# Kernel tuning notes

Measured on AMD Instinct MI355X. Metric: run time of the kernel, lower is better.

Reference implementation:

```python
import jax, jax.numpy as jnp
import numpy as np

N = 50000      # nodes
E = 800000     # edges (avg degree 16)
D_IN, D_H, D_OUT = 128, 128, 64


def setup_inputs() -> dict:
    key = jax.random.key(0)
    ks = jax.random.split(key, 12)
    s = 0.05  # weight init scale
    return {
        "x": jax.random.normal(ks[0], (N, D_IN), jnp.float32),
        "edge_index": jax.random.randint(ks[1], (2, E), 0, N, dtype=jnp.int64),
        "Wl0": jax.random.normal(ks[2], (D_H, D_IN), jnp.float32) * s,
        "bl0": jax.random.normal(ks[3], (D_H,), jnp.float32) * s,
        "Wr0": jax.random.normal(ks[4], (D_H, D_IN), jnp.float32) * s,
        "Wl1": jax.random.normal(ks[5], (D_H, D_H), jnp.float32) * s,
        "bl1": jax.random.normal(ks[6], (D_H,), jnp.float32) * s,
        "Wr1": jax.random.normal(ks[7], (D_H, D_H), jnp.float32) * s,
        "Wl2": jax.random.normal(ks[8], (D_OUT, D_H), jnp.float32) * s,
        "bl2": jax.random.normal(ks[9], (D_OUT,), jnp.float32) * s,
        "Wr2": jax.random.normal(ks[10], (D_OUT, D_H), jnp.float32) * s,
    }


def _sage_layer(h, src, dst, Wl, bl, Wr):
    # mean aggregation over incoming neighbors: out[i] = mean_{j in N(i)} h[j]
    n = h.shape[0]
    agg = jax.ops.segment_sum(h[src], dst, num_segments=n)          # [N, D]
    deg = jax.ops.segment_sum(jnp.ones((src.shape[0],), h.dtype), dst,
                              num_segments=n)                        # [N]
    mean = agg / jnp.maximum(deg, 1.0)[:, None]  # empty rows -> 0, matches torch_sparse
    # lin_l(agg) + lin_r(self); lin_r has no bias in PyG SAGEConv
    return mean @ Wl.T + bl + h @ Wr.T


def reference(x, edge_index, Wl0, bl0, Wr0, Wl1, bl1, Wr1, Wl2, bl2, Wr2):
    src, dst = edge_index[1], edge_index[0]  # adj row = dst, col = src
    h = jax.nn.relu(_sage_layer(x, src, dst, Wl0, bl0, Wr0))
    h = jax.nn.relu(_sage_layer(h, src, dst, Wl1, bl1, Wr1))
    h = _sage_layer(h, src, dst, Wl2, bl2, Wr2)
    return jax.nn.log_softmax(h, axis=1)
```

## Files before the change

kernel.cpp:

```cpp
#include <hip/hip_runtime.h>
#include <hip/hip_bf16.h>


typedef __attribute__((ext_vector_type(8))) short bf16x8;
typedef __attribute__((ext_vector_type(4))) float f32x4;

#define NPB 128
#define BCAP 2560
#define EPB 8192
#define EPT 32
#define CPAD 16

__device__ __forceinline__ unsigned short f2bf(float f) {
    unsigned int u = __builtin_bit_cast(unsigned int, f);
    u += 0x7fffu + ((u >> 16) & 1u);
    return (unsigned short)(u >> 16);
}
__device__ __forceinline__ float bf2f(unsigned int bits16) {
    return __builtin_bit_cast(float, bits16 << 16);
}


__global__ __launch_bounds__(256) void dist_cast_kernel(const int* __restrict__ dst,
                                                        const int* __restrict__ srcv,
                                                        int* __restrict__ gcnt,
                                                        unsigned int* __restrict__ staging,
                                                        int E, int NBc, int DB, int XB,
                                                        const float* __restrict__ x,
                                                        unsigned short* __restrict__ xbf,
                                                        const float* p0, const float* p1,
                                                        const float* p2, const float* p3,
                                                        const float* p4, const float* p5,
                                                        unsigned short* __restrict__ wbf) {
    __shared__ unsigned int stage[EPB];
    __shared__ int hist[400];
    __shared__ int lstart[400];
    __shared__ int gbase[400];
    __shared__ int scanbuf[256];
    int bid = blockIdx.x;
    int t = threadIdx.x;

    if (bid >= DB && bid < DB + XB) {
        int base = (bid - DB) * 256 + t;
        int stride = XB * 256;
        const float2* x2 = (const float2*)x;
        unsigned int* xo = (unsigned int*)xbf;
#pragma unroll
        for (int k = 0; k < 4; ++k) {
            int idx = base + k * stride;
            float2 v = x2[idx];
            xo[idx] = (unsigned int)f2bf(v.x) | ((unsigned int)f2bf(v.y) << 16);
        }
        return;
    }
    if (bid >= DB + XB) {
        int w = (bid - DB - XB) * 256 + t;
        if (w < 40960) {
            const float* src;
            int local;
            if      (w < 8192)  { src = p0; local = w; }
            else if (w < 16384) { src = p1; local = w - 8192; }
            else if (w < 24576) { src = p2; local = w - 16384; }
            else if (w < 32768) { src = p3; local = w - 24576; }
            else if (w < 36864) { src = p4; local = w - 32768; }
            else                { src = p5; local = w - 36864; }
            float2 v = ((const float2*)src)[local];
            unsigned int p = (unsigned int)f2bf(v.x) | ((unsigned int)f2bf(v.y) << 16);
            ((unsigned int*)wbf)[w] = p;
        }
        return;
    }

    int e0 = bid * EPB;
    unsigned int w[EPT];

    for (int b = t; b < NBc + 1; b += 256) hist[b] = 0;
    __syncthreads();

#pragma unroll
    for (int i = 0; i < EPT; ++i) {
        int e = e0 + i * 256 + t;
        unsigned int word = 0xFFFFFFFFu;
        if (e < E) word = ((unsigned int)dst[e] << 16) | (unsigned int)srcv[e];
        w[i] = word;
        int b = (int)(word >> 23); if (b > NBc) b = NBc;
        atomicAdd(&hist[b], 1);
    }
    __syncthreads();

    int b0 = 2 * t, b1 = 2 * t + 1;
    int h0 = (b0 <= NBc) ? hist[b0] : 0;
    int h1 = (b1 <= NBc) ? hist[b1] : 0;
    int pair = h0 + h1;
    scanbuf[t] = pair;
    __syncthreads();
    for (int off = 1; off < 256; off <<= 1) {
        int v = (t >= off) ? scanbuf[t - off] : 0;
        __syncthreads();
        scanbuf[t] += v;
        __syncthreads();
    }
    int excl = scanbuf[t] - pair;
    if (b0 <= NBc) lstart[b0] = excl;
    if (b1 <= NBc) lstart[b1] = excl + h0;
    __syncthreads();

    for (int b = t; b < NBc; b += 256) {
        int h = hist[b];
        gbase[b] = h ? atomicAdd(&gcnt[b * CPAD], h) : 0;
    }
    for (int b = t; b < NBc + 1; b += 256) hist[b] = lstart[b];
    __syncthreads();

#pragma unroll
    for (int i = 0; i < EPT; ++i) {
        unsigned int word = w[i];
        int b = (int)(word >> 23); if (b > NBc) b = NBc;
        int p = atomicAdd(&hist[b], 1);
        stage[p] = word;
    }
    __syncthreads();

    int total = lstart[NBc];
    for (int i = t; i < total; i += 256) {
        unsigned int word = stage[i];
        int b = (int)(word >> 23);
        int gpos = gbase[b] + (i - lstart[b]);
        staging[(size_t)b * BCAP + gpos] = word;
    }
}


template<int GY>
__device__ __forceinline__ void gemm_body(int mb, int y,
                                          const unsigned short* __restrict__ H,
                                          const unsigned short* __restrict__ Wl,
                                          const unsigned short* __restrict__ Wr,
                                          unsigned short* __restrict__ C, int N) {
    __shared__ unsigned short clds[4 * 32 * 68];
    const int NCOL = GY * 64;
    const int half = GY >> 1;
    int wave = threadIdx.x >> 6;
    int lane = threadIdx.x & 63;
    int l15 = lane & 15, quad = lane >> 4;
    const unsigned short* W = (y < half) ? Wl : Wr;
    int wrow0 = (y < half ? y : y - half) * 64;
    int col0 = y * 64;
    int m0 = mb * 128 + wave * 32;

    int r0 = m0 + l15;      if (r0 > N - 1) r0 = N - 1;
    int r1 = m0 + 16 + l15; if (r1 > N - 1) r1 = N - 1;
    const bf16x8* A0 = (const bf16x8*)(H + (size_t)r0 * 128);
    const bf16x8* A1 = (const bf16x8*)(H + (size_t)r1 * 128);

    f32x4 acc[2][4] = {};
#pragma unroll
    for (int ks = 0; ks < 4; ++ks) {
        int vidx = ks * 4 + quad;
        bf16x8 a0 = A0[vidx];
        bf16x8 a1 = A1[vidx];
#pragma unroll
        for (int j = 0; j < 4; ++j) {
            const bf16x8* B = (const bf16x8*)(W + (size_t)(wrow0 + j * 16 + l15) * 128);
            bf16x8 b = B[vidx];
            acc[0][j] = __builtin_amdgcn_mfma_f32_16x16x32_bf16(a0, b, acc[0][j], 0, 0, 0);
            acc[1][j] = __builtin_amdgcn_mfma_f32_16x16x32_bf16(a1, b, acc[1][j], 0, 0, 0);
        }
    }

    unsigned short* slice = clds + wave * (32 * 68);
#pragma unroll
    for (int i = 0; i < 2; ++i)
#pragma unroll
        for (int j = 0; j < 4; ++j)
#pragma unroll
            for (int r = 0; r < 4; ++r)
                slice[(i * 16 + quad * 4 + r) * 68 + j * 16 + l15] = f2bf(acc[i][j][r]);
    __syncthreads();

    int rlo = lane >> 3, j8 = lane & 7;
#pragma unroll
    for (int pass = 0; pass < 4; ++pass) {
        int row_local = pass * 8 + rlo;
        const unsigned short* p = slice + row_local * 68 + j8 * 8;
        unsigned long long lo = *(const unsigned long long*)(p);
        unsigned long long hi = *(const unsigned long long*)(p + 4);
        int row = m0 + row_local;
        if (row < N) {
            unsigned long long* q = (unsigned long long*)(C + (size_t)row * NCOL + col0 + j8 * 8);
            q[0] = lo;
            q[1] = hi;
        }
    }
}


__global__ __launch_bounds__(256) void build_gemm_kernel(const unsigned int* __restrict__ staging,
                                                         const int* __restrict__ gcnt,
                                                         int* __restrict__ row_ptr,
                                                         int* __restrict__ adj, int N, int NBc,
                                                         int gemmRows,
                                                         const unsigned short* __restrict__ H,
                                                         const unsigned short* __restrict__ Wl,
                                                         const unsigned short* __restrict__ Wr,
                                                         unsigned short* __restrict__ C) {
    __shared__ int hist[NPB];
    __shared__ int scn[NPB];
    __shared__ int wsum[4];
    int bid = blockIdx.x;
    int t = threadIdx.x;

    if (bid >= NBc) {
        int gid = bid - NBc;
        int mb = gid % gemmRows;
        int yy = gid / gemmRows;
        gemm_body<4>(mb, yy, H, Wl, Wr, C, N);
        return;
    }

    int b = bid;
    int n0 = b * NPB;
    int nb = N - n0; if (nb > NPB) nb = NPB;
    int ec = gcnt[b * CPAD];
    const unsigned int* st = staging + (size_t)b * BCAP;

    int a = 0;
    for (int j = t; j < b; j += 256) a += gcnt[j * CPAD];
#pragma unroll
    for (int off = 32; off; off >>= 1) a += __shfl_xor(a, off);
    if ((t & 63) == 0) wsum[t >> 6] = a;
    if (t < NPB) hist[t] = 0;
    __syncthreads();
    int bb = wsum[0] + wsum[1] + wsum[2] + wsum[3];

    for (int i = t; i < ec; i += 256)
        atomicAdd(&hist[(st[i] >> 16) & (NPB - 1)], 1);
    __syncthreads();

    int v = (t < NPB) ? hist[t] : 0;
    if (t < NPB) scn[t] = v;
    __syncthreads();
    for (int off = 1; off < NPB; off <<= 1) {
        int u = (t >= off && t < NPB) ? scn[t - off] : 0;
        __syncthreads();
        if (t < NPB) scn[t] += u;
        __syncthreads();
    }
    if (t < NPB) hist[t] = scn[t] - v;
    if (t < nb) row_ptr[n0 + t] = bb + (scn[t] - v);
    if (b == NBc - 1 && t == 0) row_ptr[N] = bb + ec;
    __syncthreads();

    for (int i = t; i < ec; i += 256) {
        unsigned int pk = st[i];
        int p = atomicAdd(&hist[(pk >> 16) & (NPB - 1)], 1);
        adj[bb + p] = (int)(pk & 0xffffu);
    }
}


template<int GY>
__global__ __launch_bounds__(256) void gemm_mfma_kernel(const unsigned short* __restrict__ H,
                                                        const unsigned short* __restrict__ Wl,
                                                        const unsigned short* __restrict__ Wr,
                                                        unsigned short* __restrict__ C,
                                                        int N) {
    gemm_body<GY>(blockIdx.x, blockIdx.y, H, Wl, Wr, C, N);
}


__global__ __launch_bounds__(256) void agg_relu_kernel(const unsigned short* __restrict__ C,
                                                       const int* __restrict__ row_ptr,
                                                       const int* __restrict__ adj,
                                                       const float* __restrict__ bias,
                                                       unsigned short* __restrict__ hout, int N) {
    int node = (int)((blockIdx.x * blockDim.x + threadIdx.x) >> 6);
    int lane = threadIdx.x & 63;
    if (node >= N) return;
    int g = lane >> 4;
    int c = lane & 15;
    int beg = row_ptr[node], end = row_ptr[node + 1];
    float p[8] = {};

    int e = beg;
    while (e < end) {
        int cnt = end - e; if (cnt > 64) cnt = 64;
        int ll = lane; if (ll > cnt - 1) ll = cnt - 1;
        int myidx = adj[e + ll];
        int c1 = cnt - 1;
        for (int i = 0; i < cnt; i += 16) {
            int t0 = i + g, t1 = i + 4 + g, t2 = i + 8 + g, t3 = i + 12 + g;
            int s0 = __shfl(myidx, t0 > c1 ? c1 : t0);
            int s1 = __shfl(myidx, t1 > c1 ? c1 : t1);
            int s2 = __shfl(myidx, t2 > c1 ? c1 : t2);
            int s3 = __shfl(myidx, t3 > c1 ? c1 : t3);
            float m0 = t0 < cnt ? 1.f : 0.f;
            float m1 = t1 < cnt ? 1.f : 0.f;
            float m2 = t2 < cnt ? 1.f : 0.f;
            float m3 = t3 < cnt ? 1.f : 0.f;
            bf16x8 v0 = ((const bf16x8*)(C + (size_t)s0 * 256))[c];
            bf16x8 v1 = ((const bf16x8*)(C + (size_t)s1 * 256))[c];
            bf16x8 v2 = ((const bf16x8*)(C + (size_t)s2 * 256))[c];
            bf16x8 v3 = ((const bf16x8*)(C + (size_t)s3 * 256))[c];
#pragma unroll
            for (int k = 0; k < 8; ++k) {
                p[k] += m0 * bf2f((unsigned short)v0[k]);
                p[k] += m1 * bf2f((unsigned short)v1[k]);
                p[k] += m2 * bf2f((unsigned short)v2[k]);
                p[k] += m3 * bf2f((unsigned short)v3[k]);
            }
        }
        e += cnt;
    }

#pragma unroll
    for (int k = 0; k < 8; ++k) {
        p[k] += __shfl_xor(p[k], 16);
        p[k] += __shfl_xor(p[k], 32);
    }

    int deg = end - beg;
    float inv = 1.0f / (float)(deg > 1 ? deg : 1);
    bf16x8 sv = ((const bf16x8*)(C + (size_t)node * 256))[16 + c];
    float4 b0 = ((const float4*)bias)[2 * c];
    float4 b1 = ((const float4*)bias)[2 * c + 1];
    float bb[8] = {b0.x, b0.y, b0.z, b0.w, b1.x, b1.y, b1.z, b1.w};
    bf16x8 o;
#pragma unroll
    for (int k = 0; k < 8; ++k) {
        float v = fmaxf(p[k] * inv + bb[k] + bf2f((unsigned short)sv[k]), 0.f);
        o[k] = (short)f2bf(v);
    }
    if (g == 0)
        ((bf16x8*)(hout + (size_t)node * 128))[c] = o;
}


__global__ __launch_bounds__(256) void final_kernel(const unsigned short* __restrict__ C,
                                                    const int* __restrict__ row_ptr,
                                                    const int* __restrict__ adj,
                                                    const float* __restrict__ bias,
                                                    float* __restrict__ out, int N) {
    int node = (int)((blockIdx.x * blockDim.x + threadIdx.x) >> 6);
    int lane = threadIdx.x & 63;
    if (node >= N) return;
    int g = lane >> 3;
    int c = lane & 7;
    int beg = row_ptr[node], end = row_ptr[node + 1];
    float p[8] = {};

    int e = beg;
    while (e < end) {
        int cnt = end - e; if (cnt > 64) cnt = 64;
        int ll = lane; if (ll > cnt - 1) ll = cnt - 1;
        int myidx = adj[e + ll];
        int c1 = cnt - 1;
        for (int i = 0; i < cnt; i += 16) {
            int ta = i + g, tb = i + 8 + g;
            int sa = __shfl(myidx, ta > c1 ? c1 : ta);
            int sb = __shfl(myidx, tb > c1 ? c1 : tb);
            float ma = ta < cnt ? 1.f : 0.f;
            float mb = tb < cnt ? 1.f : 0.f;
            bf16x8 va = ((const bf16x8*)(C + (size_t)sa * 128))[c];
            bf16x8 vb = ((const bf16x8*)(C + (size_t)sb * 128))[c];
#pragma unroll
            for (int k = 0; k < 8; ++k) {
                p[k] += ma * bf2f((unsigned short)va[k]);
                p[k] += mb * bf2f((unsigned short)vb[k]);
            }
        }
        e += cnt;
    }

#pragma unroll
    for (int k = 0; k < 8; ++k) {
        p[k] += __shfl_xor(p[k], 8);
        p[k] += __shfl_xor(p[k], 16);
        p[k] += __shfl_xor(p[k], 32);
    }

    int deg = end - beg;
    float inv = 1.0f / (float)(deg > 1 ? deg : 1);
    bf16x8 sv = ((const bf16x8*)(C + (size_t)node * 128))[8 + c];
    float4 b0 = ((const float4*)bias)[2 * c];
    float4 b1 = ((const float4*)bias)[2 * c + 1];
    float bb[8] = {b0.x, b0.y, b0.z, b0.w, b1.x, b1.y, b1.z, b1.w};
    float u[8];
#pragma unroll
    for (int k = 0; k < 8; ++k)
        u[k] = p[k] * inv + bb[k] + bf2f((unsigned short)sv[k]);

    float m = u[0];
#pragma unroll
    for (int k = 1; k < 8; ++k) m = fmaxf(m, u[k]);
#pragma unroll
    for (int off = 1; off < 8; off <<= 1) m = fmaxf(m, __shfl_xor(m, off));
    float se = 0.f;
#pragma unroll
    for (int k = 0; k < 8; ++k) se += __expf(u[k] - m);
#pragma unroll
    for (int off = 1; off < 8; off <<= 1) se += __shfl_xor(se, off);
    float ls = __logf(se);

    if (g == 0) {
        float4 o0 = {u[0] - m - ls, u[1] - m - ls, u[2] - m - ls, u[3] - m - ls};
        float4 o1 = {u[4] - m - ls, u[5] - m - ls, u[6] - m - ls, u[7] - m - ls};
        ((float4*)(out + (size_t)node * 64))[2 * c] = o0;
        ((float4*)(out + (size_t)node * 64))[2 * c + 1] = o1;
    }
}


extern "C" void kernel_launch(void* const* d_in, const int* in_sizes, int n_in,
                              void* d_out, int out_size, void* d_ws, size_t ws_size,
                              hipStream_t stream) {
    const float* x   = (const float*)d_in[0];
    const int*   ei  = (const int*)d_in[1];
    const float* Wl0 = (const float*)d_in[2];
    const float* bl0 = (const float*)d_in[3];
    const float* Wr0 = (const float*)d_in[4];
    const float* Wl1 = (const float*)d_in[5];
    const float* bl1 = (const float*)d_in[6];
    const float* Wr1 = (const float*)d_in[7];
    const float* Wl2 = (const float*)d_in[8];
    const float* bl2 = (const float*)d_in[9];
    const float* Wr2 = (const float*)d_in[10];
    float* out = (float*)d_out;

    const int N  = in_sizes[0] / 128;
    const int E  = in_sizes[1] / 2;
    const int NB = (N + NPB - 1) / NPB;

    char* ws = (char*)d_ws;
    auto alloc = [&](size_t bytes) {
        char* p = ws;
        ws += (bytes + 255) & ~(size_t)255;
        return p;
    };
    int*   row_ptr    = (int*)alloc((size_t)(N + 1) * 4);
    int*   adj        = (int*)alloc((size_t)E * 4);
    int*   gcnt       = (int*)alloc((size_t)NB * CPAD * 4);
    unsigned int* staging = (unsigned int*)alloc((size_t)NB * BCAP * 4);
    unsigned short* xbf = (unsigned short*)alloc((size_t)N * 128 * 2);
    unsigned short* wbf = (unsigned short*)alloc((size_t)81920 * 2);
    unsigned short* C   = (unsigned short*)alloc((size_t)N * 256 * 2);
    unsigned short* hA  = (unsigned short*)alloc((size_t)N * 128 * 2);
    unsigned short* hB  = (unsigned short*)alloc((size_t)N * 128 * 2);

    const int* dstp = ei;
    const int* srcp = ei + E;

    unsigned short* wl0 = wbf;
    unsigned short* wr0 = wbf + 16384;
    unsigned short* wl1 = wbf + 32768;
    unsigned short* wr1 = wbf + 49152;
    unsigned short* wl2 = wbf + 65536;
    unsigned short* wr2 = wbf + 73728;

    dim3 blk(256);
    int DB = (E + EPB - 1) / EPB;
    int XB = (N * 64) / (256 * 4);
    int gemmRows = (N + 127) / 128;
    int aggBlocks = (N * 64 + 255) / 256;

    hipMemsetAsync(gcnt, 0, (size_t)NB * CPAD * 4, stream);
    dist_cast_kernel<<<DB + XB + 160, blk, 0, stream>>>(dstp, srcp, gcnt, staging, E, NB,
                                                        DB, XB, x, xbf,
                                                        Wl0, Wr0, Wl1, Wr1, Wl2, Wr2, wbf);
    build_gemm_kernel<<<NB + gemmRows * 4, blk, 0, stream>>>(staging, gcnt, row_ptr, adj,
                                                             N, NB, gemmRows, xbf, wl0, wr0, C);
    agg_relu_kernel<<<aggBlocks, blk, 0, stream>>>(C, row_ptr, adj, bl0, hA, N);
    gemm_mfma_kernel<4><<<dim3(gemmRows, 4), blk, 0, stream>>>(hA, wl1, wr1, C, N);
    agg_relu_kernel<<<aggBlocks, blk, 0, stream>>>(C, row_ptr, adj, bl1, hB, N);
    gemm_mfma_kernel<2><<<dim3(gemmRows, 2), blk, 0, stream>>>(hB, wl2, wr2, C, N);
    final_kernel<<<aggBlocks, blk, 0, stream>>>(C, row_ptr, adj, bl2, out, N);
}
```

Measured before the change: 267.9 us.

## Split GEMM output into separate L/R buffers and aggregate two nodes per wave

The interleaved [N,256] GEMM output is split into two dense buffers: neighbor-projected rows (Cl) and self-projected rows (Cr). Gathered rows in the aggregation are then contiguous 256-byte rows instead of strided halves of 512-byte rows, which should improve cache-line use for random gathers. The aggregation and final kernels now process two nodes per wavefront, with interleaved loads for both, to raise memory-level parallelism and halve wave count. The cost is more register pressure and extra branching for unequal degrees.

```diff
diff --git a/kernel.cpp b/kernel.cpp
--- a/kernel.cpp
+++ b/kernel.cpp
@@ -136,16 +136,20 @@
                                           const unsigned short* __restrict__ H,
                                           const unsigned short* __restrict__ Wl,
                                           const unsigned short* __restrict__ Wr,
-                                          unsigned short* __restrict__ C, int N) {
+                                          unsigned short* __restrict__ Cl,
+                                          unsigned short* __restrict__ Cr, int N) {
     __shared__ unsigned short clds[4 * 32 * 68];
-    const int NCOL = GY * 64;
-    const int half = GY >> 1;
+    const int halfY = GY >> 1;
+    const int ldc = GY * 32;
     int wave = threadIdx.x >> 6;
     int lane = threadIdx.x & 63;
     int l15 = lane & 15, quad = lane >> 4;
-    const unsigned short* W = (y < half) ? Wl : Wr;
-    int wrow0 = (y < half ? y : y - half) * 64;
-    int col0 = y * 64;
+    bool isL = y < halfY;
+    const unsigned short* W = isL ? Wl : Wr;
+    unsigned short* Cp = isL ? Cl : Cr;
+    int yy = isL ? y : y - halfY;
+    int wrow0 = yy * 64;
+    int col0 = yy * 64;
     int m0 = mb * 128 + wave * 32;
 
     int r0 = m0 + l15;      if (r0 > N - 1) r0 = N - 1;
@@ -187,7 +191,7 @@
         unsigned long long hi = *(const unsigned long long*)(p + 4);
         int row = m0 + row_local;
         if (row < N) {
-            unsigned long long* q = (unsigned long long*)(C + (size_t)row * NCOL + col0 + j8 * 8);
+            unsigned long long* q = (unsigned long long*)(Cp + (size_t)row * ldc + col0 + j8 * 8);
             q[0] = lo;
             q[1] = hi;
         }
@@ -203,7 +207,8 @@
                                                          const unsigned short* __restrict__ H,
                                                          const unsigned short* __restrict__ Wl,
                                                          const unsigned short* __restrict__ Wr,
-                                                         unsigned short* __restrict__ C) {
+                                                         unsigned short* __restrict__ Cl,
+                                                         unsigned short* __restrict__ Cr) {
     __shared__ int hist[NPB];
     __shared__ int scn[NPB];
     __shared__ int wsum[4];
@@ -214,7 +219,7 @@
         int gid = bid - NBc;
         int mb = gid % gemmRows;
         int yy = gid / gemmRows;
-        gemm_body<4>(mb, yy, H, Wl, Wr, C, N);
+        gemm_body<4>(mb, yy, H, Wl, Wr, Cl, Cr, N);
         return;
     }
 
@@ -263,150 +268,287 @@
 __global__ __launch_bounds__(256) void gemm_mfma_kernel(const unsigned short* __restrict__ H,
                                                         const unsigned short* __restrict__ Wl,
                                                         const unsigned short* __restrict__ Wr,
-                                                        unsigned short* __restrict__ C,
+                                                        unsigned short* __restrict__ Cl,
+                                                        unsigned short* __restrict__ Cr,
                                                         int N) {
-    gemm_body<GY>(blockIdx.x, blockIdx.y, H, Wl, Wr, C, N);
-}
-
-
-__global__ __launch_bounds__(256) void agg_relu_kernel(const unsigned short* __restrict__ C,
+    gemm_body<GY>(blockIdx.x, blockIdx.y, Wl ? H : H, Wl, Wr, Cl, Cr, N);
+}
+
+
+__global__ __launch_bounds__(256) void agg_relu_kernel(const unsigned short* __restrict__ Cl,
+                                                       const unsigned short* __restrict__ Cr,
                                                        const int* __restrict__ row_ptr,
                                                        const int* __restrict__ adj,
                                                        const float* __restrict__ bias,
                                                        unsigned short* __restrict__ hout, int N) {
-    int node = (int)((blockIdx.x * blockDim.x + threadIdx.x) >> 6);
+    int pr = (int)((blockIdx.x * blockDim.x + threadIdx.x) >> 6);
     int lane = threadIdx.x & 63;
-    if (node >= N) return;
-    int g = lane >> 4;
-    int c = lane & 15;
-    int beg = row_ptr[node], end = row_ptr[node + 1];
-    float p[8] = {};
-
-    int e = beg;
-    while (e < end) {
-        int cnt = end - e; if (cnt > 64) cnt = 64;
-        int ll = lane; if (ll > cnt - 1) ll = cnt - 1;
-        int myidx = adj[e + ll];
+    int nodeA = pr * 2;
+    if (nodeA >= N) return;
+    int nodeB = nodeA + 1;
+    bool hasB = nodeB < N;
+    int g = lane >> 4, c = lane & 15;
+    int begA = row_ptr[nodeA], endA = row_ptr[nodeA + 1];
+    int begB = hasB ? row_ptr[nodeB] : 0;
+    int endB = hasB ? row_ptr[nodeB + 1] : 0;
+    float pA[8] = {}, pB[8] = {};
+
+    int cntA = endA - begA; if (cntA > 64) cntA = 64;
+    int cntB = endB - begB; if (cntB > 64) cntB = 64;
+    int idxA = (cntA > 0) ? adj[begA + (lane < cntA ? lane : cntA - 1)] : 0;
+    int idxB = (cntB > 0) ? adj[begB + (lane < cntB ? lane : cntB - 1)] : 0;
+    int c1A = cntA - 1, c1B = cntB - 1;
+    int mx = cntA > cntB ? cntA : cntB;
+    for (int i = 0; i < mx; i += 16) {
+        bool doA = i < cntA, doB = i < cntB;
+        bf16x8 vA[4], vB[4];
+        float mA[4], mB[4];
+        if (doA) {
+#pragma unroll
+            for (int s = 0; s < 4; ++s) {
+                int tt = i + s * 4 + g;
+                int src = __shfl(idxA, tt > c1A ? c1A : tt);
+                mA[s] = tt < cntA ? 1.f : 0.f;
+                vA[s] = ((const bf16x8*)(Cl + (size_t)src * 128))[c];
+            }
+        }
+        if (doB) {
+#pragma unroll
+            for (int s = 0; s < 4; ++s) {
+                int tt = i + s * 4 + g;
+                int src = __shfl(idxB, tt > c1B ? c1B : tt);
+                mB[s] = tt < cntB ? 1.f : 0.f;
+                vB[s] = ((const bf16x8*)(Cl + (size_t)src * 128))[c];
+            }
+        }
+        if (doA) {
+#pragma unroll
+            for (int s = 0; s < 4; ++s)
+#pragma unroll
+                for (int k = 0; k < 8; ++k)
+                    pA[k] += mA[s] * bf2f((unsigned short)vA[s][k]);
+        }
+        if (doB) {
+#pragma unroll
+            for (int s = 0; s < 4; ++s)
+#pragma unroll
+                for (int k = 0; k < 8; ++k)
+                    pB[k] += mB[s] * bf2f((unsigned short)vB[s][k]);
+        }
+    }
+    for (int e = begA + 64; e < endA; e += 64) {
+        int cnt = endA - e; if (cnt > 64) cnt = 64;
+        int idx = adj[e + (lane < cnt ? lane : cnt - 1)];
         int c1 = cnt - 1;
         for (int i = 0; i < cnt; i += 16) {
-            int t0 = i + g, t1 = i + 4 + g, t2 = i + 8 + g, t3 = i + 12 + g;
-            int s0 = __shfl(myidx, t0 > c1 ? c1 : t0);
-            int s1 = __shfl(myidx, t1 > c1 ? c1 : t1);
-            int s2 = __shfl(myidx, t2 > c1 ? c1 : t2);
-            int s3 = __shfl(myidx, t3 > c1 ? c1 : t3);
-            float m0 = t0 < cnt ? 1.f : 0.f;
-            float m1 = t1 < cnt ? 1.f : 0.f;
-            float m2 = t2 < cnt ? 1.f : 0.f;
-            float m3 = t3 < cnt ? 1.f : 0.f;
-            bf16x8 v0 = ((const bf16x8*)(C + (size_t)s0 * 256))[c];
-            bf16x8 v1 = ((const bf16x8*)(C + (size_t)s1 * 256))[c];
-            bf16x8 v2 = ((const bf16x8*)(C + (size_t)s2 * 256))[c];
-            bf16x8 v3 = ((const bf16x8*)(C + (size_t)s3 * 256))[c];
-#pragma unroll
-            for (int k = 0; k < 8; ++k) {
-                p[k] += m0 * bf2f((unsigned short)v0[k]);
-                p[k] += m1 * bf2f((unsigned short)v1[k]);
-                p[k] += m2 * bf2f((unsigned short)v2[k]);
-                p[k] += m3 * bf2f((unsigned short)v3[k]);
-            }
-        }
-        e += cnt;
+#pragma unroll
+            for (int s = 0; s < 4; ++s) {
+                int tt = i + s * 4 + g;
+                int src = __shfl(idx, tt > c1 ? c1 : tt);
+                float m = tt < cnt ? 1.f : 0.f;
+                bf16x8 v = ((const bf16x8*)(Cl + (size_t)src * 128))[c];
+#pragma unroll
+                for (int k = 0; k < 8; ++k)
+                    pA[k] += m * bf2f((unsigned short)v[k]);
+            }
+        }
+    }
+    for (int e = begB + 64; e < endB; e += 64) {
+        int cnt = endB - e; if (cnt > 64) cnt = 64;
+        int idx = adj[e + (lane < cnt ? lane : cnt - 1)];
+        int c1 = cnt - 1;
+        for (int i = 0; i < cnt; i += 16) {
+#pragma unroll
+            for (int s = 0; s < 4; ++s) {
+                int tt = i + s * 4 + g;
+                int src = __shfl(idx, tt > c1 ? c1 : tt);
+                float m = tt < cnt ? 1.f : 0.f;
+                bf16x8 v = ((const bf16x8*)(Cl + (size_t)src * 128))[c];
+#pragma unroll
+                for (int k = 0; k < 8; ++k)
+                    pB[k] += m * bf2f((unsigned short)v[k]);
+            }
+        }
     }
 
 #pragma unroll
     for (int k = 0; k < 8; ++k) {
-        p[k] += __shfl_xor(p[k], 16);
-        p[k] += __shfl_xor(p[k], 32);
-    }
-
-    int deg = end - beg;
-    float inv = 1.0f / (float)(deg > 1 ? deg : 1);
-    bf16x8 sv = ((const bf16x8*)(C + (size_t)node * 256))[16 + c];
+        pA[k] += __shfl_xor(pA[k], 16);
+        pA[k] += __shfl_xor(pA[k], 32);
+        pB[k] += __shfl_xor(pB[k], 16);
+        pB[k] += __shfl_xor(pB[k], 32);
+    }
+
+    int degA = endA - begA, degB = endB - begB;
+    float invA = 1.0f / (float)(degA > 1 ? degA : 1);
+    float invB = 1.0f / (float)(degB > 1 ? degB : 1);
+    bf16x8 svA = ((const bf16x8*)(Cr + (size_t)nodeA * 128))[c];
+    bf16x8 svB = hasB ? ((const bf16x8*)(Cr + (size_t)nodeB * 128))[c] : svA;
     float4 b0 = ((const float4*)bias)[2 * c];
     float4 b1 = ((const float4*)bias)[2 * c + 1];
     float bb[8] = {b0.x, b0.y, b0.z, b0.w, b1.x, b1.y, b1.z, b1.w};
-    bf16x8 o;
+    bf16x8 oA, oB;
 #pragma unroll
     for (int k = 0; k < 8; ++k) {
-        float v = fmaxf(p[k] * inv + bb[k] + bf2f((unsigned short)sv[k]), 0.f);
-        o[k] = (short)f2bf(v);
+        oA[k] = (short)f2bf(fmaxf(pA[k] * invA + bb[k] + bf2f((unsigned short)svA[k]), 0.f));
+        oB[k] = (short)f2bf(fmaxf(pB[k] * invB + bb[k] + bf2f((unsigned short)svB[k]), 0.f));
     }
     if (g == 0)
-        ((bf16x8*)(hout + (size_t)node * 128))[c] = o;
-}
-
-
-__global__ __launch_bounds__(256) void final_kernel(const unsigned short* __restrict__ C,
+        ((bf16x8*)(hout + (size_t)nodeA * 128))[c] = oA;
+    else if (g == 1 && hasB)
+        ((bf16x8*)(hout + (size_t)nodeB * 128))[c] = oB;
+}
+
+
+__global__ __launch_bounds__(256) void final_kernel(const unsigned short* __restrict__ Cl2,
+                                                    const unsigned short* __restrict__ Cr2,
                                                     const int* __restrict__ row_ptr,
                                                     const int* __restrict__ adj,
                                                     const float* __restrict__ bias,
                                                     float* __restrict__ out, int N) {
-    int node = (int)((blockIdx.x * blockDim.x + threadIdx.x) >> 6);
+    int pr = (int)((blockIdx.x * blockDim.x + threadIdx.x) >> 6);
     int lane = threadIdx.x & 63;
-    if (node >= N) return;
-    int g = lane >> 3;
-    int c = lane & 7;
-    int beg = row_ptr[node], end = row_ptr[node + 1];
-    float p[8] = {};
-
-    int e = beg;
-    while (e < end) {
-        int cnt = end - e; if (cnt > 64) cnt = 64;
-        int ll = lane; if (ll > cnt - 1) ll = cnt - 1;
-        int myidx = adj[e + ll];
+    int nodeA = pr * 2;
+    if (nodeA >= N) return;
+    int nodeB = nodeA + 1;
+    bool hasB = nodeB < N;
+    int g = lane >> 3, c = lane & 7;
+    int begA = row_ptr[nodeA], endA = row_ptr[nodeA + 1];
+    int begB = hasB ? row_ptr[nodeB] : 0;
+    int endB = hasB ? row_ptr[nodeB + 1] : 0;
+    float pA[8] = {}, pB[8] = {};
+
+    int cntA = endA - begA; if (cntA > 64) cntA = 64;
+    int cntB = endB - begB; if (cntB > 64) cntB = 64;
+    int idxA = (cntA > 0) ? adj[begA + (lane < cntA ? lane : cntA - 1)] : 0;
+    int idxB = (cntB > 0) ? adj[begB + (lane < cntB ? lane : cntB - 1)] : 0;
+    int c1A = cntA - 1, c1B = cntB - 1;
+    int mx = cntA > cntB ? cntA : cntB;
+    for (int i = 0; i < mx; i += 16) {
+        bool doA = i < cntA, doB = i < cntB;
+        bf16x8 vA[2], vB[2];
+        float mA[2], mB[2];
+        if (doA) {
+#pragma unroll
+            for (int s = 0; s < 2; ++s) {
+                int tt = i + s * 8 + g;
+                int src = __shfl(idxA, tt > c1A ? c1A : tt);
+                mA[s] = tt < cntA ? 1.f : 0.f;
+                vA[s] = ((const bf16x8*)(Cl2 + (size_t)src * 64))[c];
+            }
+        }
+        if (doB) {
+#pragma unroll
+            for (int s = 0; s < 2; ++s) {
+                int tt = i + s * 8 + g;
+                int src = __shfl(idxB, tt > c1B ? c1B : tt);
+                mB[s] = tt < cntB ? 1.f : 0.f;
+                vB[s] = ((const bf16x8*)(Cl2 + (size_t)src * 64))[c];
+            }
+        }
+        if (doA) {
+#pragma unroll
+            for (int s = 0; s < 2; ++s)
+#pragma unroll
+                for (int k = 0; k < 8; ++k)
+                    pA[k] += mA[s] * bf2f((unsigned short)vA[s][k]);
+        }
+        if (doB) {
+#pragma unroll
+            for (int s = 0; s < 2; ++s)
+#pragma unroll
+                for (int k = 0; k < 8; ++k)
+                    pB[k] += mB[s] * bf2f((unsigned short)vB[s][k]);
+        }
+    }
+    for (int e = begA + 64; e < endA; e += 64) {
+        int cnt = endA - e; if (cnt > 64) cnt = 64;
+        int idx = adj[e + (lane < cnt ? lane : cnt - 1)];
         int c1 = cnt - 1;
         for (int i = 0; i < cnt; i += 16) {
-            int ta = i + g, tb = i + 8 + g;
-            int sa = __shfl(myidx, ta > c1 ? c1 : ta);
-            int sb = __shfl(myidx, tb > c1 ? c1 : tb);
-            float ma = ta < cnt ? 1.f : 0.f;
-            float mb = tb < cnt ? 1.f : 0.f;
-            bf16x8 va = ((const bf16x8*)(C + (size_t)sa * 128))[c];
-            bf16x8 vb = ((const bf16x8*)(C + (size_t)sb * 128))[c];
-#pragma unroll
-            for (int k = 0; k < 8; ++k) {
-                p[k] += ma * bf2f((unsigned short)va[k]);
-                p[k] += mb * bf2f((unsigned short)vb[k]);
-            }
-        }
-        e += cnt;
+#pragma unroll
+            for (int s = 0; s < 2; ++s) {
+                int tt = i + s * 8 + g;
+                int src = __shfl(idx, tt > c1 ? c1 : tt);
+                float m = tt < cnt ? 1.f : 0.f;
+                bf16x8 v = ((const bf16x8*)(Cl2 + (size_t)src * 64))[c];
+#pragma unroll
+                for (int k = 0; k < 8; ++k)
+                    pA[k] += m * bf2f((unsigned short)v[k]);
+            }
+        }
+    }
+    for (int e = begB + 64; e < endB; e += 64) {
+        int cnt = endB - e; if (cnt > 64) cnt = 64;
+        int idx = adj[e + (lane < cnt ? lane : cnt - 1)];
+        int c1 = cnt - 1;
+        for (int i = 0; i < cnt; i += 16) {
+#pragma unroll
+            for (int s = 0; s < 2; ++s) {
+                int tt = i + s * 8 + g;
+                int src = __shfl(idx, tt > c1 ? c1 : tt);
+                float m = tt < cnt ? 1.f : 0.f;
+                bf16x8 v = ((const bf16x8*)(Cl2 + (size_t)src * 64))[c];
+#pragma unroll
+                for (int k = 0; k < 8; ++k)
+                    pB[k] += m * bf2f((unsigned short)v[k]);
+            }
+        }
     }
 
 #pragma unroll
     for (int k = 0; k < 8; ++k) {
-        p[k] += __shfl_xor(p[k], 8);
-        p[k] += __shfl_xor(p[k], 16);
-        p[k] += __shfl_xor(p[k], 32);
-    }
-
-    int deg = end - beg;
-    float inv = 1.0f / (float)(deg > 1 ? deg : 1);
-    bf16x8 sv = ((const bf16x8*)(C + (size_t)node * 128))[8 + c];
+        pA[k] += __shfl_xor(pA[k], 8);
+        pA[k] += __shfl_xor(pA[k], 16);
+        pA[k] += __shfl_xor(pA[k], 32);
+        pB[k] += __shfl_xor(pB[k], 8);
+        pB[k] += __shfl_xor(pB[k], 16);
+        pB[k] += __shfl_xor(pB[k], 32);
+    }
+
+    int degA = endA - begA, degB = endB - begB;
+    float invA = 1.0f / (float)(degA > 1 ? degA : 1);
+    float invB = 1.0f / (float)(degB > 1 ? degB : 1);
+    bf16x8 svA = ((const bf16x8*)(Cr2 + (size_t)nodeA * 64))[c];
+    bf16x8 svB = hasB ? ((const bf16x8*)(Cr2 + (size_t)nodeB * 64))[c] : svA;
     float4 b0 = ((const float4*)bias)[2 * c];
     float4 b1 = ((const float4*)bias)[2 * c + 1];
     float bb[8] = {b0.x, b0.y, b0.z, b0.w, b1.x, b1.y, b1.z, b1.w};
-    float u[8];
-#pragma unroll
-    for (int k = 0; k < 8; ++k)
-        u[k] = p[k] * inv + bb[k] + bf2f((unsigned short)sv[k]);
-
-    float m = u[0];
-#pragma unroll
-    for (int k = 1; k < 8; ++k) m = fmaxf(m, u[k]);
-#pragma unroll
-    for (int off = 1; off < 8; off <<= 1) m = fmaxf(m, __shfl_xor(m, off));
-    float se = 0.f;
-#pragma unroll
-    for (int k = 0; k < 8; ++k) se += __expf(u[k] - m);
-#pragma unroll
-    for (int off = 1; off < 8; off <<= 1) se += __shfl_xor(se, off);
-    float ls = __logf(se);
+    float uA[8], uB[8];
+#pragma unroll
+    for (int k = 0; k < 8; ++k) {
+        uA[k] = pA[k] * invA + bb[k] + bf2f((unsigned short)svA[k]);
+        uB[k] = pB[k] * invB + bb[k] + bf2f((unsigned short)svB[k]);
+    }
+
+    float mA_ = uA[0], mB_ = uB[0];
+#pragma unroll
+    for (int k = 1; k < 8; ++k) { mA_ = fmaxf(mA_, uA[k]); mB_ = fmaxf(mB_, uB[k]); }
+#pragma unroll
+    for (int off = 1; off < 8; off <<= 1) {
+        mA_ = fmaxf(mA_, __shfl_xor(mA_, off));
+        mB_ = fmaxf(mB_, __shfl_xor(mB_, off));
+    }
+    float seA = 0.f, seB = 0.f;
+#pragma unroll
+    for (int k = 0; k < 8; ++k) { seA += __expf(uA[k] - mA_); seB += __expf(uB[k] - mB_); }
+#pragma unroll
+    for (int off = 1; off < 8; off <<= 1) {
+        seA += __shfl_xor(seA, off);
+        seB += __shfl_xor(seB, off);
+    }
+    float lsA = __logf(seA), lsB = __logf(seB);
 
     if (g == 0) {
-        float4 o0 = {u[0] - m - ls, u[1] - m - ls, u[2] - m - ls, u[3] - m - ls};
-        float4 o1 = {u[4] - m - ls, u[5] - m - ls, u[6] - m - ls, u[7] - m - ls};
-        ((float4*)(out + (size_t)node * 64))[2 * c] = o0;
-        ((float4*)(out + (size_t)node * 64))[2 * c + 1] = o1;
+        float4 o0 = {uA[0] - mA_ - lsA, uA[1] - mA_ - lsA, uA[2] - mA_ - lsA, uA[3] - mA_ - lsA};
+        float4 o1 = {uA[4] - mA_ - lsA, uA[5] - mA_ - lsA, uA[6] - mA_ - lsA, uA[7] - mA_ - lsA};
+        ((float4*)(out + (size_t)nodeA * 64))[2 * c] = o0;
+        ((float4*)(out + (size_t)nodeA * 64))[2 * c + 1] = o1;
+    } else if (g == 1 && hasB) {
+        float4 o0 = {uB[0] - mB_ - lsB, uB[1] - mB_ - lsB, uB[2] - mB_ - lsB, uB[3] - mB_ - lsB};
+        float4 o1 = {uB[4] - mB_ - lsB, uB[5] - mB_ - lsB, uB[6] - mB_ - lsB, uB[7] - mB_ - lsB};
+        ((float4*)(out + (size_t)nodeB * 64))[2 * c] = o0;
+        ((float4*)(out + (size_t)nodeB * 64))[2 * c + 1] = o1;
     }
 }
 
@@ -439,11 +581,12 @@
     };
     int*   row_ptr    = (int*)alloc((size_t)(N + 1) * 4);
     int*   adj        = (int*)alloc((size_t)E * 4);
-    int*   gcnt       = (int*)alloc((size_t)NB * CPAD * 4);
+    int*   gcnt      = (int*)alloc((size_t)NB * CPAD * 4);
     unsigned int* staging = (unsigned int*)alloc((size_t)NB * BCAP * 4);
     unsigned short* xbf = (unsigned short*)alloc((size_t)N * 128 * 2);
     unsigned short* wbf = (unsigned short*)alloc((size_t)81920 * 2);
-    unsigned short* C   = (unsigned short*)alloc((size_t)N * 256 * 2);
+    unsigned short* Cl  = (unsigned short*)alloc((size_t)N * 128 * 2);
+    unsigned short* Cr  = (unsigned short*)alloc((size_t)N * 128 * 2);
     unsigned short* hA  = (unsigned short*)alloc((size_t)N * 128 * 2);
     unsigned short* hB  = (unsigned short*)alloc((size_t)N * 128 * 2);
 
@@ -461,17 +604,18 @@
     int DB = (E + EPB - 1) / EPB;
     int XB = (N * 64) / (256 * 4);
     int gemmRows = (N + 127) / 128;
-    int aggBlocks = (N * 64 + 255) / 256;
+    int pairBlocks = (((N + 1) / 2) * 64 + 255) / 256;
 
     hipMemsetAsync(gcnt, 0, (size_t)NB * CPAD * 4, stream);
     dist_cast_kernel<<<DB + XB + 160, blk, 0, stream>>>(dstp, srcp, gcnt, staging, E, NB,
                                                         DB, XB, x, xbf,
                                                         Wl0, Wr0, Wl1, Wr1, Wl2, Wr2, wbf);
     build_gemm_kernel<<<NB + gemmRows * 4, blk, 0, stream>>>(staging, gcnt, row_ptr, adj,
-                                                             N, NB, gemmRows, xbf, wl0, wr0, C);
-    agg_relu_kernel<<<aggBlocks, blk, 0, stream>>>(C, row_ptr, adj, bl0, hA, N);
-    gemm_mfma_kernel<4><<<dim3(gemmRows, 4), blk, 0, stream>>>(hA, wl1, wr1, C, N);
-    agg_relu_kernel<<<aggBlocks, blk, 0, stream>>>(C, row_ptr, adj, bl1, hB, N);
-    gemm_mfma_kernel<2><<<dim3(gemmRows, 2), blk, 0, stream>>>(hB, wl2, wr2, C, N);
-    final_kernel<<<aggBlocks, blk, 0, stream>>>(C, row_ptr, adj, bl2, out, N);
-}
+                                                             N, NB, gemmRows, xbf, wl0, wr0,
+                                                             Cl, Cr);
+    agg_relu_kernel<<<pairBlocks, blk, 0, stream>>>(Cl, Cr, row_ptr, adj, bl0, hA, N);
+    gemm_mfma_kernel<4><<<dim3(gemmRows, 4), blk, 0, stream>>>(hA, wl1, wr1, Cl, Cr, N);
+    agg_relu_kernel<<<pairBlocks, blk, 0, stream>>>(Cl, Cr, row_ptr, adj, bl1, hB, N);
+    gemm_mfma_kernel<2><<<dim3(gemmRows, 2), blk, 0, stream>>>(hB, wl2, wr2, Cl, Cr, N);
+    final_kernel<<<pairBlocks, blk, 0, stream>>>(Cl, Cr, row_ptr, adj, bl2, out, N);
+}
```

New measurement: 273.3 us. 1.02x slower.
